# Kernel optimization log

Hardware: AMD Instinct MI355X
Metric: run time of the kernel (lower is better)

## Reference

```python
import jax, jax.numpy as jnp
import numpy as np

H = 256  # hidden size
I = 2    # input size / output size


def setup_inputs() -> dict:
    key = jax.random.key(0)
    ks = jax.random.split(key, 11)
    s1 = 1.0 / np.sqrt(H)
    u = lambda k, shape: jax.random.uniform(k, shape, jnp.float32, -s1, s1)
    return {
        "inputs": jax.random.normal(ks[0], (512, 256, I), jnp.float32),
        "W_ih1": u(ks[1], (4 * H, I)),
        "W_hh1": u(ks[2], (4 * H, H)),
        "b_ih1": u(ks[3], (4 * H,)),
        "b_hh1": u(ks[4], (4 * H,)),
        "W_ih2": u(ks[5], (4 * H, H)),
        "W_hh2": u(ks[6], (4 * H, H)),
        "b_ih2": u(ks[7], (4 * H,)),
        "b_hh2": u(ks[8], (4 * H,)),
        "W_lin": u(ks[9], (I, H)),
        "b_lin": u(ks[10], (I,)),
    }


def _lstm_cell(x, h, c, W_ih, W_hh, b_ih, b_hh):
    # PyTorch LSTMCell gate order: i, f, g, o
    gates = x @ W_ih.T + b_ih + h @ W_hh.T + b_hh  # (B, 4H)
    i, f, g, o = jnp.split(gates, 4, axis=-1)
    c_new = jax.nn.sigmoid(f) * c + jax.nn.sigmoid(i) * jnp.tanh(g)
    h_new = jax.nn.sigmoid(o) * jnp.tanh(c_new)
    return h_new, c_new


def reference(inputs, W_ih1, W_hh1, b_ih1, b_hh1, W_ih2, W_hh2, b_ih2, b_hh2,
              W_lin, b_lin):
    B = inputs.shape[0]
    xs = jnp.transpose(inputs, (1, 0, 2))  # (T, B, I)
    zeros = jnp.zeros((B, H), inputs.dtype)
    carry0 = (zeros, zeros, zeros, zeros)

    def step(carry, x_t):
        h1, c1, h2, c2 = carry
        # NOTE: the original clones/masks x_t into lstm_input_t but never
        # uses it — the cell consumes raw input_t, so we do the same.
        h1, c1 = _lstm_cell(x_t, h1, c1, W_ih1, W_hh1, b_ih1, b_hh1)
        h2, c2 = _lstm_cell(h1, h2, c2, W_ih2, W_hh2, b_ih2, b_hh2)
        y = h2 @ W_lin.T + b_lin  # (B, I)
        return (h1, c1, h2, c2), y

    _, ys = jax.lax.scan(step, carry0, xs)  # ys: (T, B, I)
    return jnp.transpose(ys, (1, 0, 2))  # (B, T, I)
```

## Files before the change

### kernel.cpp

```cpp
#include <hip/hip_runtime.h>


typedef float vf2 __attribute__((ext_vector_type(2)));
typedef float v4f __attribute__((ext_vector_type(4)));
typedef _Float16 vh4 __attribute__((ext_vector_type(4)));
typedef _Float16 vh8 __attribute__((ext_vector_type(8)));

#define NT 512
#define TSTEPS 256
#define NSA 128
#define NSB 8
#define NVPF 40
#define NLPF 16
#define FRB 1024
#define SBBASE (1024 * FRB)
#define VPBASE (1088 * FRB)
#define LPBASE (1408 * FRB)
#define FS 393216

__global__ void prep_kernel(const float* __restrict__ W_ih1,
                            const float* __restrict__ W_hh1,
                            const float* __restrict__ b_ih1,
                            const float* __restrict__ b_hh1,
                            const float* __restrict__ W_ih2,
                            const float* __restrict__ W_hh2,
                            const float* __restrict__ b_ih2,
                            const float* __restrict__ b_hh2,
                            void* __restrict__ ws) {
    const int stride = gridDim.x * blockDim.x;
    const int idx = blockIdx.x * blockDim.x + threadIdx.x;
    _Float16* wh = (_Float16*)ws;
    float* wf = (float*)ws;
    for (int e = idx; e < 786432; e += stride) {
        int kb = e >> 9;
        int lane = (e & 511) >> 3, jj = e & 7;
        int w, rt, kt, m;
        if (kb < 1024) {
            w = kb >> 7; int f = kb & 127;
            if (f < 64) { m = 0; rt = f >> 3;       kt = f & 7; }
            else        { m = 1; rt = (f >> 3) & 7; kt = f & 7; }
        } else if (kb < 1088) {
            int k1 = kb - 1024; w = k1 >> 3; m = 2; rt = k1 & 7; kt = 0;
        } else if (kb < 1408) {
            int k2 = kb - 1088; w = k2 / 40; int p = k2 % 40;
            m = 2; rt = p / 5; kt = 1 + p % 5;
        } else {
            int k3 = kb - 1408; w = k3 >> 4; int q = k3 & 15;
            m = 2; rt = q >> 1; kt = 6 + (q & 1);
        }
        int row = w * 128 + rt * 16 + (lane & 15);
        int k   = kt * 32 + ((lane >> 4) << 3) + jj;
        float v = (m == 0) ? W_hh1[row * 256 + k]
                : (m == 1) ? W_ih2[row * 256 + k]
                           : W_hh2[row * 256 + k];
        wh[e] = (_Float16)v;
    }
    for (int j = idx; j < 1024; j += stride) {
        wf[FS + j]        = W_ih1[j * 2 + 0];
        wf[FS + 1024 + j] = W_ih1[j * 2 + 1];
        wf[FS + 2048 + j] = b_ih1[j] + b_hh1[j];
        wf[FS + 3072 + j] = b_ih2[j] + b_hh2[j];
    }
}

__device__ __forceinline__ float sig_(float v) {
    return 1.f / (1.f + __expf(-v));
}
__device__ __forceinline__ float tanh_(float v) {
    return 1.f - 2.f / (__expf(2.f * v) + 1.f);
}
__device__ __forceinline__ v4f mfma16(vh8 a, vh8 b, v4f c) {
    return __builtin_amdgcn_mfma_f32_16x16x32_f16(a, b, c, 0, 0, 0);
}

#define BARRIER() __asm__ volatile("s_waitcnt lgkmcnt(0)\ns_barrier" ::: "memory")

__global__ __launch_bounds__(NT, 2) void lstm_kernel(
    const float* __restrict__ x,
    const void* __restrict__ ws,
    const float* __restrict__ W_lin,
    const float* __restrict__ b_lin,
    float* __restrict__ out)
{
    __shared__ float g1buf[2][1024];
    __shared__ float g2buf[2][1024];
    __shared__ __align__(16) _Float16 h1s[2][256];
    __shared__ __align__(16) _Float16 h2s[2][256];
    __shared__ __align__(16) char lds_park[NLPF * 8 * FRB];

    const int tid = threadIdx.x;
    const int lane = tid & 63, w = tid >> 6;
    const int u = tid & 255, bu = tid >> 8;
    const int b0 = blockIdx.x * 2;
    const char* wstream = (const char*)ws;
    const float* wf = (const float*)ws;
    const int l16 = lane * 16;

    float wxa[4], wxb[4], b1c[4], b2c[4];
    #pragma unroll
    for (int g = 0; g < 4; ++g) {
        int r = g * 256 + u;
        wxa[g] = wf[FS + r];        wxb[g] = wf[FS + 1024 + r];
        b1c[g] = wf[FS + 2048 + r]; b2c[g] = wf[FS + 3072 + r];
    }

    const int ob = (w >> 1) & 1, oo = w & 1;
    const float wl0 = W_lin[oo * 256 + 4 * lane + 0];
    const float wl1 = W_lin[oo * 256 + 4 * lane + 1];
    const float wl2 = W_lin[oo * 256 + 4 * lane + 2];
    const float wl3 = W_lin[oo * 256 + 4 * lane + 3];
    const float blin = b_lin[oo];

    ((_Float16*)h1s)[tid] = (_Float16)0.f;
    ((_Float16*)h2s)[tid] = (_Float16)0.f;
    g1buf[0][tid] = 0.f; g1buf[0][512 + tid] = 0.f;
    g1buf[1][tid] = 0.f; g1buf[1][512 + tid] = 0.f;

    float c1 = 0.f, c2 = 0.f;

    for (int q = 0; q < NLPF; ++q) {
        *(vh8*)&lds_park[(((q << 3) + w) << 10) + l16] =
            *(const vh8*)(wstream + LPBASE + (((w << 4) + q) << 10) + l16);
    }

    vh8 wreg[NVPF];
    #pragma unroll
    for (int p = 0; p < NVPF; ++p) {
        union { vh8 v; float f[4]; } tpk;
        tpk.v = *(const vh8*)(wstream + VPBASE + ((w * NVPF + p) << 10) + l16);
        asm volatile("" : "+v"(tpk.f[0]), "+v"(tpk.f[1]),
                          "+v"(tpk.f[2]), "+v"(tpk.f[3]));
        wreg[p] = tpk.v;
    }

    const char* wbaseA = wstream + (size_t)w * (NSA * FRB);
    const char* wbaseB = wstream + SBBASE + (size_t)w * (NSB * FRB);
    int spA = 0, spB = 0;
    vh8 B0, B1, B2, B3, B4, B5, B6, B7, E0, E1;
    auto LDA = [&](vh8& d) {
        d = *(const vh8*)(wbaseA + spA + l16);
        spA += FRB; if (spA == NSA * FRB) spA = 0;
    };
    auto LDB = [&](vh8& d) {
        d = *(const vh8*)(wbaseB + spB + l16);
        spB += FRB; if (spB == NSB * FRB) spB = 0;
    };
    LDA(B0); LDA(B1); LDA(B2); LDA(B3);
    LDA(B4); LDA(B5); LDA(B6); LDA(B7);
    LDB(E0); LDB(E1);

    auto bfrag = [&](const _Float16 (*hp)[256], int kt) -> vh8 {
        return *(const vh8*)&hp[lane & 1][kt * 32 + ((lane >> 4) << 3)];
    };

    const int bx = b0 + bu;
    vf2 xv = *(const vf2*)(x + (size_t)bx * 512);

    __syncthreads();

    #pragma unroll 1
    for (int t = 0; t < TSTEPS; ++t) {
        {
            float p0 = g1buf[bu][u]       + b1c[0] + wxa[0] * xv.x + wxb[0] * xv.y;
            float p1 = g1buf[bu][256 + u] + b1c[1] + wxa[1] * xv.x + wxb[1] * xv.y;
            float p2 = g1buf[bu][512 + u] + b1c[2] + wxa[2] * xv.x + wxb[2] * xv.y;
            float p3 = g1buf[bu][768 + u] + b1c[3] + wxa[3] * xv.x + wxb[3] * xv.y;
            c1 = sig_(p1) * c1 + sig_(p0) * tanh_(p2);
            h1s[bu][u] = (_Float16)(sig_(p3) * tanh_(c1));
        }
        {
            const int tn = (t + 1) & (TSTEPS - 1);
            xv = *(const vf2*)(x + (size_t)bx * 512 + tn * 2);
        }
        BARRIER();

        if (t > 0 && w < 4) {
            vh4 hv = *(const vh4*)&h2s[ob][4 * lane];
            float s = (float)hv.x * wl0 + (float)hv.y * wl1
                    + (float)hv.z * wl2 + (float)hv.w * wl3;
            #pragma unroll
            for (int m = 32; m >= 1; m >>= 1) s += __shfl_xor(s, m, 64);
            if (lane == 0)
                out[(size_t)(b0 + ob) * 512 + (t - 1) * 2 + oo] = s + blin;
        }

        #pragma unroll 1
        for (int rt = 0; rt < 8; ++rt) {
            v4f acc = {0.f, 0.f, 0.f, 0.f};
            acc = mfma16(B0, bfrag(h1s, 0), acc); LDA(B0);
            acc = mfma16(B1, bfrag(h1s, 1), acc); LDA(B1);
            acc = mfma16(B2, bfrag(h1s, 2), acc); LDA(B2);
            acc = mfma16(B3, bfrag(h1s, 3), acc); LDA(B3);
            acc = mfma16(B4, bfrag(h1s, 4), acc); LDA(B4);
            acc = mfma16(B5, bfrag(h1s, 5), acc); LDA(B5);
            acc = mfma16(B6, bfrag(h1s, 6), acc); LDA(B6);
            acc = mfma16(B7, bfrag(h1s, 7), acc); LDA(B7);
            if ((lane & 15) < 2)
                *(v4f*)&g1buf[lane & 15][w * 128 + rt * 16 + ((lane >> 4) << 2)] = acc;
        }

        #pragma unroll 1
        for (int rt = 0; rt < 8; ++rt) {
            v4f acc = {0.f, 0.f, 0.f, 0.f};
            acc = mfma16(B0, bfrag(h1s, 0), acc); LDA(B0);
            acc = mfma16(B1, bfrag(h1s, 1), acc); LDA(B1);
            acc = mfma16(B2, bfrag(h1s, 2), acc); LDA(B2);
            acc = mfma16(B3, bfrag(h1s, 3), acc); LDA(B3);
            acc = mfma16(B4, bfrag(h1s, 4), acc); LDA(B4);
            acc = mfma16(B5, bfrag(h1s, 5), acc); LDA(B5);
            acc = mfma16(B6, bfrag(h1s, 6), acc); LDA(B6);
            acc = mfma16(B7, bfrag(h1s, 7), acc); LDA(B7);
            if ((lane & 15) < 2)
                *(v4f*)&g2buf[lane & 15][w * 128 + rt * 16 + ((lane >> 4) << 2)] = acc;
        }

        #pragma unroll
        for (int rt = 0; rt < 8; ++rt) {
            v4f acc = {0.f, 0.f, 0.f, 0.f};
            if ((lane & 15) < 2)
                acc = *(const v4f*)&g2buf[lane & 15][w * 128 + rt * 16 + ((lane >> 4) << 2)];
            if (rt & 1) { acc = mfma16(E1, bfrag(h2s, 0), acc); LDB(E1); }
            else        { acc = mfma16(E0, bfrag(h2s, 0), acc); LDB(E0); }
            acc = mfma16(wreg[rt * 5 + 0], bfrag(h2s, 1), acc);
            acc = mfma16(wreg[rt * 5 + 1], bfrag(h2s, 2), acc);
            acc = mfma16(wreg[rt * 5 + 2], bfrag(h2s, 3), acc);
            acc = mfma16(wreg[rt * 5 + 3], bfrag(h2s, 4), acc);
            acc = mfma16(wreg[rt * 5 + 4], bfrag(h2s, 5), acc);
            {
                vh8 A6 = *(const vh8*)
                    &lds_park[((((rt * 2 + 0) << 3) + w) << 10) + l16];
                acc = mfma16(A6, bfrag(h2s, 6), acc);
            }
            {
                vh8 A7 = *(const vh8*)
                    &lds_park[((((rt * 2 + 1) << 3) + w) << 10) + l16];
                acc = mfma16(A7, bfrag(h2s, 7), acc);
            }
            if ((lane & 15) < 2)
                *(v4f*)&g2buf[lane & 15][w * 128 + rt * 16 + ((lane >> 4) << 2)] = acc;
        }
        BARRIER();

        {
            float q0 = g2buf[bu][u]       + b2c[0];
            float q1 = g2buf[bu][256 + u] + b2c[1];
            float q2 = g2buf[bu][512 + u] + b2c[2];
            float q3 = g2buf[bu][768 + u] + b2c[3];
            c2 = sig_(q1) * c2 + sig_(q0) * tanh_(q2);
            h2s[bu][u] = (_Float16)(sig_(q3) * tanh_(c2));
        }
    }

    BARRIER();
    if (w < 4) {
        vh4 hv = *(const vh4*)&h2s[ob][4 * lane];
        float s = (float)hv.x * wl0 + (float)hv.y * wl1
                + (float)hv.z * wl2 + (float)hv.w * wl3;
        #pragma unroll
        for (int m = 32; m >= 1; m >>= 1) s += __shfl_xor(s, m, 64);
        if (lane == 0)
            out[(size_t)(b0 + ob) * 512 + 255 * 2 + oo] = s + blin;
    }
}

extern "C" void kernel_launch(void* const* d_in, const int* in_sizes, int n_in,
                              void* d_out, int out_size, void* d_ws, size_t ws_size,
                              hipStream_t stream) {
    const float* x     = (const float*)d_in[0];
    const float* W_ih1 = (const float*)d_in[1];
    const float* W_hh1 = (const float*)d_in[2];
    const float* b_ih1 = (const float*)d_in[3];
    const float* b_hh1 = (const float*)d_in[4];
    const float* W_ih2 = (const float*)d_in[5];
    const float* W_hh2 = (const float*)d_in[6];
    const float* b_ih2 = (const float*)d_in[7];
    const float* b_hh2 = (const float*)d_in[8];
    const float* W_lin = (const float*)d_in[9];
    const float* b_lin = (const float*)d_in[10];
    float* out = (float*)d_out;

    prep_kernel<<<256, 256, 0, stream>>>(W_ih1, W_hh1, b_ih1, b_hh1,
                                         W_ih2, W_hh2, b_ih2, b_hh2, d_ws);
    lstm_kernel<<<256, NT, 0, stream>>>(x, d_ws, W_lin, b_lin, out);
}
```

Measured before the change: 3.368 ms.

## Merge weight streams into one ring and stream more W_hh2 fragments

Merges the two streamed weight rings (the W_hh1/W_ih2 ring and the small W_hh2 column-0 ring) into a single per-wave stream of 144 fragments. W_hh2 k-tiles 0 and 5 now come from that stream through the same rotating B0-B7 registers, and the register-resident fragments drop from 40 to 32. This frees eight vh8 registers plus the separate E0/E1 buffers and the second pointer bookkeeping. The cost is more global/L2 streaming traffic per timestep in the layer-2 recurrent matmul.

Result: faster. 2.705 ms (-19.7%).

```diff
diff --git a/kernel.cpp b/kernel.cpp
--- a/kernel.cpp
+++ b/kernel.cpp
@@ -8,13 +8,11 @@
 
 #define NT 512
 #define TSTEPS 256
-#define NSA 128
-#define NSB 8
-#define NVPF 40
+#define NSF 144
+#define NVPF 32
 #define NLPF 16
 #define FRB 1024
-#define SBBASE (1024 * FRB)
-#define VPBASE (1088 * FRB)
+#define VPBASE (1152 * FRB)
 #define LPBASE (1408 * FRB)
 #define FS 393216
 
@@ -35,15 +33,14 @@
         int kb = e >> 9;
         int lane = (e & 511) >> 3, jj = e & 7;
         int w, rt, kt, m;
-        if (kb < 1024) {
-            w = kb >> 7; int f = kb & 127;
-            if (f < 64) { m = 0; rt = f >> 3;       kt = f & 7; }
-            else        { m = 1; rt = (f >> 3) & 7; kt = f & 7; }
-        } else if (kb < 1088) {
-            int k1 = kb - 1024; w = k1 >> 3; m = 2; rt = k1 & 7; kt = 0;
+        if (kb < 1152) {
+            w = kb / 144; int f = kb % 144;
+            if (f < 64)       { m = 0; rt = f >> 3;        kt = f & 7; }
+            else if (f < 128) { m = 1; rt = (f - 64) >> 3; kt = f & 7; }
+            else { int q = f - 128; m = 2; rt = q >> 1; kt = (q & 1) ? 5 : 0; }
         } else if (kb < 1408) {
-            int k2 = kb - 1088; w = k2 / 40; int p = k2 % 40;
-            m = 2; rt = p / 5; kt = 1 + p % 5;
+            int p2 = kb - 1152; w = p2 >> 5; int p = p2 & 31;
+            m = 2; rt = p >> 2; kt = 1 + (p & 3);
         } else {
             int k3 = kb - 1408; w = k3 >> 4; int q = k3 & 15;
             m = 2; rt = q >> 1; kt = 6 + (q & 1);
@@ -133,21 +130,15 @@
         wreg[p] = tpk.v;
     }
 
-    const char* wbaseA = wstream + (size_t)w * (NSA * FRB);
-    const char* wbaseB = wstream + SBBASE + (size_t)w * (NSB * FRB);
-    int spA = 0, spB = 0;
-    vh8 B0, B1, B2, B3, B4, B5, B6, B7, E0, E1;
+    const char* wbase = wstream + (size_t)w * (NSF * FRB);
+    int sp = 0;
+    vh8 B0, B1, B2, B3, B4, B5, B6, B7;
     auto LDA = [&](vh8& d) {
-        d = *(const vh8*)(wbaseA + spA + l16);
-        spA += FRB; if (spA == NSA * FRB) spA = 0;
-    };
-    auto LDB = [&](vh8& d) {
-        d = *(const vh8*)(wbaseB + spB + l16);
-        spB += FRB; if (spB == NSB * FRB) spB = 0;
+        d = *(const vh8*)(wbase + sp + l16);
+        sp += FRB; if (sp == NSF * FRB) sp = 0;
     };
     LDA(B0); LDA(B1); LDA(B2); LDA(B3);
     LDA(B4); LDA(B5); LDA(B6); LDA(B7);
-    LDB(E0); LDB(E1);
 
     auto bfrag = [&](const _Float16 (*hp)[256], int kt) -> vh8 {
         return *(const vh8*)&hp[lane & 1][kt * 32 + ((lane >> 4) << 3)];
@@ -214,31 +205,35 @@
                 *(v4f*)&g2buf[lane & 15][w * 128 + rt * 16 + ((lane >> 4) << 2)] = acc;
         }
 
-        #pragma unroll
-        for (int rt = 0; rt < 8; ++rt) {
-            v4f acc = {0.f, 0.f, 0.f, 0.f};
-            if ((lane & 15) < 2)
-                acc = *(const v4f*)&g2buf[lane & 15][w * 128 + rt * 16 + ((lane >> 4) << 2)];
-            if (rt & 1) { acc = mfma16(E1, bfrag(h2s, 0), acc); LDB(E1); }
-            else        { acc = mfma16(E0, bfrag(h2s, 0), acc); LDB(E0); }
-            acc = mfma16(wreg[rt * 5 + 0], bfrag(h2s, 1), acc);
-            acc = mfma16(wreg[rt * 5 + 1], bfrag(h2s, 2), acc);
-            acc = mfma16(wreg[rt * 5 + 2], bfrag(h2s, 3), acc);
-            acc = mfma16(wreg[rt * 5 + 3], bfrag(h2s, 4), acc);
-            acc = mfma16(wreg[rt * 5 + 4], bfrag(h2s, 5), acc);
-            {
-                vh8 A6 = *(const vh8*)
-                    &lds_park[((((rt * 2 + 0) << 3) + w) << 10) + l16];
-                acc = mfma16(A6, bfrag(h2s, 6), acc);
-            }
-            {
-                vh8 A7 = *(const vh8*)
-                    &lds_park[((((rt * 2 + 1) << 3) + w) << 10) + l16];
-                acc = mfma16(A7, bfrag(h2s, 7), acc);
-            }
-            if ((lane & 15) < 2)
-                *(v4f*)&g2buf[lane & 15][w * 128 + rt * 16 + ((lane >> 4) << 2)] = acc;
-        }
+#define P2B(RT, BA, BB)                                                        \
+        {                                                                      \
+            v4f acc = {0.f, 0.f, 0.f, 0.f};                                    \
+            if ((lane & 15) < 2)                                               \
+                acc = *(const v4f*)&g2buf[lane & 15]                           \
+                        [w * 128 + RT * 16 + ((lane >> 4) << 2)];              \
+            acc = mfma16(BA, bfrag(h2s, 0), acc); LDA(BA);                     \
+            acc = mfma16(wreg[RT * 4 + 0], bfrag(h2s, 1), acc);                \
+            acc = mfma16(wreg[RT * 4 + 1], bfrag(h2s, 2), acc);                \
+            acc = mfma16(wreg[RT * 4 + 2], bfrag(h2s, 3), acc);                \
+            acc = mfma16(wreg[RT * 4 + 3], bfrag(h2s, 4), acc);                \
+            acc = mfma16(BB, bfrag(h2s, 5), acc); LDA(BB);                     \
+            {                                                                  \
+                vh8 A6 = *(const vh8*)                                         \
+                    &lds_park[((((RT * 2 + 0) << 3) + w) << 10) + l16];        \
+                acc = mfma16(A6, bfrag(h2s, 6), acc);                          \
+            }                                                                  \
+            {                                                                  \
+                vh8 A7 = *(const vh8*)                                         \
+                    &lds_park[((((RT * 2 + 1) << 3) + w) << 10) + l16];        \
+                acc = mfma16(A7, bfrag(h2s, 7), acc);                          \
+            }                                                                  \
+            if ((lane & 15) < 2)                                               \
+                *(v4f*)&g2buf[lane & 15]                                       \
+                    [w * 128 + RT * 16 + ((lane >> 4) << 2)] = acc;            \
+        }
+        P2B(0, B0, B1) P2B(1, B2, B3) P2B(2, B4, B5) P2B(3, B6, B7)
+        P2B(4, B0, B1) P2B(5, B2, B3) P2B(6, B4, B5) P2B(7, B6, B7)
+#undef P2B
         BARRIER();
 
         {
```
